# Optimization experiments

Hardware: AMD Instinct MI355X
Metric: run time of the kernel (lower is better)

The kernel has to match this reference:

```python
import jax, jax.numpy as jnp
import numpy as np

N_NODES = 100000
N_EDGES = 1600000
IN_DIM, HID_DIM, OUT_DIM = 128, 64, 64


def setup_inputs() -> dict:
    key = jax.random.key(0)
    ks = jax.random.split(key, 8)
    x = jax.random.normal(ks[0], (N_NODES, IN_DIM), dtype=jnp.float32)
    edge_index = jax.random.randint(ks[1], (2, N_EDGES), 0, N_NODES, dtype=jnp.int32)
    edge_weight = jax.random.uniform(ks[2], (N_EDGES,), dtype=jnp.float32)
    # GCNConv parameters (glorot-ish init)
    w1 = jax.random.normal(ks[3], (IN_DIM, HID_DIM), dtype=jnp.float32) / np.sqrt(IN_DIM)
    b1 = jnp.zeros((HID_DIM,), dtype=jnp.float32)
    w2 = jax.random.normal(ks[4], (HID_DIM, OUT_DIM), dtype=jnp.float32) / np.sqrt(HID_DIM)
    b2 = jnp.zeros((OUT_DIM,), dtype=jnp.float32)
    return {"x": x, "edge_index": edge_index, "edge_weight": edge_weight,
            "w1": w1, "b1": b1, "w2": w2, "b2": b2}


def _gcn_conv(h, src, dst, edge_weight, w, b, n_nodes):
    # GCNConv(normalize=False): linear transform, then edge-weighted scatter-add
    # (source_to_target flow: gather from src, scatter-sum into dst), then bias.
    h = h @ w                                   # [N, out]
    msg = h[src] * edge_weight[:, None]          # [E, out] irregular gather
    agg = jax.ops.segment_sum(msg, dst, num_segments=n_nodes)  # [N, out]
    return agg + b


def reference(x, edge_index, edge_weight, w1, b1, w2, b2):
    src, dst = edge_index[0], edge_index[1]
    n = x.shape[0]
    # Dropout is identity in eval mode (training=False).
    h = _gcn_conv(x, src, dst, edge_weight, w1, b1, n)
    h = jax.nn.relu(h)
    out = _gcn_conv(h, src, dst, edge_weight, w2, b2, n)
    return out
```

## Files before the change

kernel.cpp:

```cpp
#include <hip/hip_runtime.h>
#include <hip/hip_bf16.h>


#define N_NODES 100000
#define N_EDGES 1600000
#define NB1     391
#define T1      4096
#define NT1     391
#define EPT     8
#define CAP1    4706
#define GB1     782

typedef unsigned short ushort_t;
typedef unsigned int uint_t;
typedef __attribute__((ext_vector_type(8))) short bf16x8;
typedef __attribute__((ext_vector_type(4))) float floatx4;
typedef __attribute__((ext_vector_type(8))) ushort_t ushort8v;

static __device__ __forceinline__ float bf2f(ushort_t h) {
    return __uint_as_float(((uint_t)h) << 16);
}
static __device__ __forceinline__ ushort_t f2bf(float f) {
    uint_t u = __float_as_uint(f);
    u = (u + 0x7FFF + ((u >> 16) & 1)) >> 16;
    return (ushort_t)u;
}

__global__ __launch_bounds__(512) void k_init(int* __restrict__ gcursor)
{
    int t = threadIdx.x;
    if (t < NB1) gcursor[t] = t * CAP1;
}

__global__ __launch_bounds__(512) void k_p1g1(
    const int* __restrict__ src, const int* __restrict__ dst,
    const float* __restrict__ ew, int* __restrict__ gcursor,
    int2* __restrict__ recs1, int E,
    const float* __restrict__ X, const float* __restrict__ W,
    ushort_t* __restrict__ Y, int N)
{
    __shared__ __align__(16) char smem[47296];
    const int tid = threadIdx.x;

    if (blockIdx.x < NT1) {
        int* cnt     = (int*)smem;
        int* start   = cnt + NB1;
        int* cursor  = start + NB1;
        int* gb      = cursor + NB1;
        int* wsum    = (int*)(smem + 6256);
        int* wexc    = wsum + 8;
        int2* stg    = (int2*)(smem + 6336);
        ushort_t* sb = (ushort_t*)(smem + 39104);
        const int t = tid, b = blockIdx.x;
        const int lane = t & 63, wv = t >> 6;

        int   rd[EPT]; int rs[EPT]; float rw[EPT];
        const int e0 = b * T1;
        const int e1 = min(E, e0 + T1);
        #pragma unroll
        for (int i = 0; i < EPT; ++i) {
            int e  = e0 + t + i * 512;
            int ee = (e < e1) ? e : e0;
            rd[i] = dst[ee];
            rs[i] = src[ee];
            rw[i] = ew[ee];
            if (e >= e1) rd[i] = -1;
        }

        if (t < NB1) cnt[t] = 0;
        __syncthreads();
        #pragma unroll
        for (int i = 0; i < EPT; ++i)
            if (rd[i] >= 0) atomicAdd(&cnt[rd[i] >> 8], 1);
        __syncthreads();

        const int v = (t < NB1) ? cnt[t] : 0;
        int x = v;
        #pragma unroll
        for (int off = 1; off < 64; off <<= 1) {
            int y = __shfl_up(x, off);
            if (lane >= off) x += y;
        }
        if (lane == 63) wsum[wv] = x;
        __syncthreads();
        if (t < 8) {
            int w  = wsum[t];
            int xx = w;
            #pragma unroll
            for (int off = 1; off < 8; off <<= 1) {
                int y = __shfl_up(xx, off);
                if (t >= off) xx += y;
            }
            wexc[t] = xx - w;
        }
        __syncthreads();
        if (t < NB1) {
            int st = x + wexc[wv] - v;
            start[t]  = st;
            cursor[t] = st;
            gb[t]     = atomicAdd(&gcursor[t], v);
        }
        __syncthreads();

        #pragma unroll
        for (int i = 0; i < EPT; ++i) {
            int d = rd[i];
            if (d >= 0) {
                int bk = d >> 8;
                int p  = atomicAdd(&cursor[bk], 1);
                int2 r;
                r.x = ((d & 255) << 17) | rs[i];
                r.y = __float_as_int(rw[i]);
                stg[p] = r;
                sb[p]  = (ushort_t)bk;
            }
        }
        __syncthreads();
        const int n = e1 - e0;
        for (int i = t; i < n; i += 512) {
            int bk = sb[i];
            recs1[gb[bk] + (i - start[bk])] = stg[i];
        }
    } else {
        ushort_t* sA = (ushort_t*)smem;
        ushort_t* sB = (ushort_t*)(smem + 18432);
        const int b    = blockIdx.x - NT1;
        const int row0 = b * 128;

        for (int i = tid; i < 128 * 16; i += 512) {
            int k = i >> 4, n4 = (i & 15) * 4;
            float4 v = *(const float4*)(W + (size_t)k * 64 + n4);
            sB[(n4 + 0) * 136 + k] = f2bf(v.x);
            sB[(n4 + 1) * 136 + k] = f2bf(v.y);
            sB[(n4 + 2) * 136 + k] = f2bf(v.z);
            sB[(n4 + 3) * 136 + k] = f2bf(v.w);
        }
        for (int i = tid; i < 128 * 16; i += 512) {
            int r = i >> 4, c4 = (i & 15) * 4;
            int rg = row0 + r; if (rg > N - 1) rg = N - 1;
            float4 v = *(const float4*)(X + (size_t)rg * 128 + c4);
            *(ushort4*)(sA + r * 72 + c4) =
                make_ushort4(f2bf(v.x), f2bf(v.y), f2bf(v.z), f2bf(v.w));
        }
        __syncthreads();

        const int wid = tid >> 6, lane = tid & 63;
        const int m = lane & 15, quad = lane >> 4;
        floatx4 acc[4] = {};

        #pragma unroll
        for (int ksl = 0; ksl < 2; ++ksl) {
            bf16x8 a = *(const bf16x8*)(sA + (wid * 16 + m) * 72 + ksl * 32 + quad * 8);
            #pragma unroll
            for (int nt = 0; nt < 4; ++nt) {
                bf16x8 bfr = *(const bf16x8*)(sB + (nt * 16 + m) * 136 + ksl * 32 + quad * 8);
                acc[nt] = __builtin_amdgcn_mfma_f32_16x16x32_bf16(a, bfr, acc[nt], 0, 0, 0);
            }
        }
        __syncthreads();
        for (int i = tid; i < 128 * 16; i += 512) {
            int r = i >> 4, c4 = (i & 15) * 4;
            int rg = row0 + r; if (rg > N - 1) rg = N - 1;
            float4 v = *(const float4*)(X + (size_t)rg * 128 + 64 + c4);
            *(ushort4*)(sA + r * 72 + c4) =
                make_ushort4(f2bf(v.x), f2bf(v.y), f2bf(v.z), f2bf(v.w));
        }
        __syncthreads();
        #pragma unroll
        for (int ksl = 0; ksl < 2; ++ksl) {
            bf16x8 a = *(const bf16x8*)(sA + (wid * 16 + m) * 72 + ksl * 32 + quad * 8);
            #pragma unroll
            for (int nt = 0; nt < 4; ++nt) {
                bf16x8 bfr = *(const bf16x8*)(sB + (nt * 16 + m) * 136 + 64 + ksl * 32 + quad * 8);
                acc[nt] = __builtin_amdgcn_mfma_f32_16x16x32_bf16(a, bfr, acc[nt], 0, 0, 0);
            }
        }
        __syncthreads();
        #pragma unroll
        for (int nt = 0; nt < 4; ++nt)
            #pragma unroll
            for (int r = 0; r < 4; ++r)
                sA[(wid * 16 + quad * 4 + r) * 72 + nt * 16 + m] = f2bf(acc[nt][r]);
        __syncthreads();
        for (int i = tid; i < 128 * 8; i += 512) {
            int rr = i >> 3, c8 = (i & 7) * 8;
            int rg = row0 + rr;
            if (rg < N)
                *(ushort8v*)(Y + (size_t)rg * 64 + c8) =
                    *(const ushort8v*)(sA + rr * 72 + c8);
        }
    }
}

__global__ __launch_bounds__(1024) void k_pass2(
    const int2* __restrict__ recs1, const int* __restrict__ gcursor,
    int2* __restrict__ recs2, int2* __restrict__ nodeinfo, int N)
{
    __shared__ int cnt[256];
    __shared__ int s[256];
    __shared__ int cursor[256];
    const int t = threadIdx.x, b = blockIdx.x;
    const int lo = b * CAP1;
    const int hi = gcursor[b];

    if (t < 256) cnt[t] = 0;
    __syncthreads();
    for (int j = lo + t; j < hi; j += 1024)
        atomicAdd(&cnt[((uint_t)recs1[j].x) >> 17], 1);
    __syncthreads();
    const int v = (t < 256) ? cnt[t] : 0;
    if (t < 256) s[t] = v;
    #pragma unroll
    for (int off = 1; off < 256; off <<= 1) {
        __syncthreads();
        int a = (t >= off && t < 256) ? s[t - off] : 0;
        __syncthreads();
        if (t < 256) s[t] += a;
    }
    __syncthreads();
    if (t < 256) {
        const int stl = s[t] - v;
        cursor[t] = stl;
        const int ng = b * 256 + t;
        if (ng < N) {
            int2 ni; ni.x = lo + stl; ni.y = v;
            nodeinfo[ng] = ni;
        }
    }
    __syncthreads();
    for (int j = lo + t; j < hi; j += 1024) {
        int2 r = recs1[j];
        int dl = ((uint_t)r.x) >> 17;
        int p  = atomicAdd(&cursor[dl], 1);
        int2 o;
        o.x = r.x & 0x1FFFF;
        o.y = r.y;
        recs2[lo + p] = o;
    }
}

__global__ __launch_bounds__(256) void k_gather_mm(
    const ushort_t* __restrict__ H, const int2* __restrict__ recs,
    const int2* __restrict__ nodeinfo, const float* __restrict__ bias1,
    const float* __restrict__ W2, ushort_t* __restrict__ out)
{
    __shared__ ushort_t sW[64 * 72];
    __shared__ ushort_t strip[4][128];

    const int tid  = threadIdx.x;
    const int wid  = tid >> 6;
    const int lane = tid & 63;
    const int n0   = (blockIdx.x * 4 + wid) * 2;
    const int n1   = n0 + 1;

    for (int i = tid; i < 64 * 16; i += 256) {
        int k = i >> 4, n4 = (i & 15) * 4;
        float4 v = *(const float4*)(W2 + (size_t)k * 64 + n4);
        sW[(n4 + 0) * 72 + k] = f2bf(v.x);
        sW[(n4 + 1) * 72 + k] = f2bf(v.y);
        sW[(n4 + 2) * 72 + k] = f2bf(v.z);
        sW[(n4 + 3) * 72 + k] = f2bf(v.w);
    }

    const int2 niA = nodeinfo[n0];
    const int2 niB = nodeinfo[n1];
    int baseA = niA.x; const int endA = niA.x + niA.y;
    int baseB = niB.x; const int endB = niB.x + niB.y;

    const int g  = lane >> 4;
    const int c4 = (lane & 15) * 4;

    float a0 = 0.f, a1 = 0.f, a2 = 0.f, a3 = 0.f;
    float b0 = 0.f, b1 = 0.f, b2 = 0.f, b3 = 0.f;

    while (baseA < endA || baseB < endB) {
        int mA = endA - baseA; if (mA > 64) mA = 64;
        int mB = endB - baseB; if (mB > 64) mB = 64;
        int2 rA = (mA > 0) ? recs[baseA + (lane < mA ? lane : mA - 1)]
                           : make_int2(0, 0);
        int2 rB = (mB > 0) ? recs[baseB + (lane < mB ? lane : mB - 1)]
                           : make_int2(0, 0);
        float wAf = __int_as_float(rA.y);
        float wBf = __int_as_float(rB.y);
        int mm = mA > mB ? mA : mB;
        #pragma unroll 4
        for (int jj = 0; jj < mm; jj += 4) {
            int idx = jj + g;
            int   sA_ = __shfl(rA.x, idx);
            float wA  = __shfl(wAf, idx);
            int   sB_ = __shfl(rB.x, idx);
            float wB  = __shfl(wBf, idx);
            if (idx >= mA) wA = 0.f;
            if (idx >= mB) wB = 0.f;
            ushort4 hA = *(const ushort4*)(H + (size_t)sA_ * 64 + c4);
            ushort4 hB = *(const ushort4*)(H + (size_t)sB_ * 64 + c4);
            a0 = fmaf(wA, bf2f(hA.x), a0);
            a1 = fmaf(wA, bf2f(hA.y), a1);
            a2 = fmaf(wA, bf2f(hA.z), a2);
            a3 = fmaf(wA, bf2f(hA.w), a3);
            b0 = fmaf(wB, bf2f(hB.x), b0);
            b1 = fmaf(wB, bf2f(hB.y), b1);
            b2 = fmaf(wB, bf2f(hB.z), b2);
            b3 = fmaf(wB, bf2f(hB.w), b3);
        }
        baseA += 64;
        baseB += 64;
    }
    a0 += __shfl_down(a0, 32); a1 += __shfl_down(a1, 32);
    a2 += __shfl_down(a2, 32); a3 += __shfl_down(a3, 32);
    b0 += __shfl_down(b0, 32); b1 += __shfl_down(b1, 32);
    b2 += __shfl_down(b2, 32); b3 += __shfl_down(b3, 32);
    a0 += __shfl_down(a0, 16); a1 += __shfl_down(a1, 16);
    a2 += __shfl_down(a2, 16); a3 += __shfl_down(a3, 16);
    b0 += __shfl_down(b0, 16); b1 += __shfl_down(b1, 16);
    b2 += __shfl_down(b2, 16); b3 += __shfl_down(b3, 16);

    if (lane < 16) {
        float4 bv = *(const float4*)(bias1 + c4);
        float vA0 = fmaxf(a0 + bv.x, 0.f), vA1 = fmaxf(a1 + bv.y, 0.f);
        float vA2 = fmaxf(a2 + bv.z, 0.f), vA3 = fmaxf(a3 + bv.w, 0.f);
        float vB0 = fmaxf(b0 + bv.x, 0.f), vB1 = fmaxf(b1 + bv.y, 0.f);
        float vB2 = fmaxf(b2 + bv.z, 0.f), vB3 = fmaxf(b3 + bv.w, 0.f);
        *(ushort4*)(&strip[wid][0 * 64 + c4]) =
            make_ushort4(f2bf(vA0), f2bf(vA1), f2bf(vA2), f2bf(vA3));
        *(ushort4*)(&strip[wid][1 * 64 + c4]) =
            make_ushort4(f2bf(vB0), f2bf(vB1), f2bf(vB2), f2bf(vB3));
    }
    __syncthreads();

    const int m = lane & 15, quad = lane >> 4;
    const ushort_t* sp = strip[wid];
    floatx4 acc2[4] = {};
    #pragma unroll
    for (int ks = 0; ks < 2; ++ks) {
        bf16x8 a = *(const bf16x8*)(sp + (m & 1) * 64 + ks * 32 + quad * 8);
        #pragma unroll
        for (int nt = 0; nt < 4; ++nt) {
            bf16x8 bfr = *(const bf16x8*)(sW + (nt * 16 + m) * 72 + ks * 32 + quad * 8);
            acc2[nt] = __builtin_amdgcn_mfma_f32_16x16x32_bf16(a, bfr, acc2[nt], 0, 0, 0);
        }
    }
    if (quad == 0) {
        #pragma unroll
        for (int nt = 0; nt < 4; ++nt) {
            strip[wid][0 * 64 + nt * 16 + m] = f2bf(acc2[nt][0]);
            strip[wid][1 * 64 + nt * 16 + m] = f2bf(acc2[nt][1]);
        }
    }
    __syncthreads();
    if (lane < 32) {
        int rr = lane >> 4, mm2 = lane & 15;
        *(ushort4*)(out + (size_t)(n0 + rr) * 64 + mm2 * 4) =
            *(const ushort4*)(&strip[wid][rr * 64 + mm2 * 4]);
    }
}

__global__ __launch_bounds__(256) void k_gather2(
    const ushort_t* __restrict__ H, const int2* __restrict__ recs,
    const int2* __restrict__ nodeinfo, const float* __restrict__ bias,
    float* __restrict__ out)
{
    const int wid  = threadIdx.x >> 6;
    const int lane = threadIdx.x & 63;
    const int n0   = (blockIdx.x * 4 + wid) * 2;
    const int n1   = n0 + 1;

    const int2 niA = nodeinfo[n0];
    const int2 niB = nodeinfo[n1];
    int baseA = niA.x; const int endA = niA.x + niA.y;
    int baseB = niB.x; const int endB = niB.x + niB.y;

    const int g  = lane >> 4;
    const int c4 = (lane & 15) * 4;

    float a0 = 0.f, a1 = 0.f, a2 = 0.f, a3 = 0.f;
    float b0 = 0.f, b1 = 0.f, b2 = 0.f, b3 = 0.f;

    while (baseA < endA || baseB < endB) {
        int mA = endA - baseA; if (mA > 64) mA = 64;
        int mB = endB - baseB; if (mB > 64) mB = 64;
        int2 rA = (mA > 0) ? recs[baseA + (lane < mA ? lane : mA - 1)]
                           : make_int2(0, 0);
        int2 rB = (mB > 0) ? recs[baseB + (lane < mB ? lane : mB - 1)]
                           : make_int2(0, 0);
        float wAf = __int_as_float(rA.y);
        float wBf = __int_as_float(rB.y);
        int mm = mA > mB ? mA : mB;
        #pragma unroll 4
        for (int jj = 0; jj < mm; jj += 4) {
            int idx = jj + g;
            int   sA_ = __shfl(rA.x, idx);
            float wA  = __shfl(wAf, idx);
            int   sB_ = __shfl(rB.x, idx);
            float wB  = __shfl(wBf, idx);
            if (idx >= mA) wA = 0.f;
            if (idx >= mB) wB = 0.f;
            ushort4 hA = *(const ushort4*)(H + (size_t)sA_ * 64 + c4);
            ushort4 hB = *(const ushort4*)(H + (size_t)sB_ * 64 + c4);
            a0 = fmaf(wA, bf2f(hA.x), a0);
            a1 = fmaf(wA, bf2f(hA.y), a1);
            a2 = fmaf(wA, bf2f(hA.z), a2);
            a3 = fmaf(wA, bf2f(hA.w), a3);
            b0 = fmaf(wB, bf2f(hB.x), b0);
            b1 = fmaf(wB, bf2f(hB.y), b1);
            b2 = fmaf(wB, bf2f(hB.z), b2);
            b3 = fmaf(wB, bf2f(hB.w), b3);
        }
        baseA += 64;
        baseB += 64;
    }
    a0 += __shfl_down(a0, 32); a1 += __shfl_down(a1, 32);
    a2 += __shfl_down(a2, 32); a3 += __shfl_down(a3, 32);
    b0 += __shfl_down(b0, 32); b1 += __shfl_down(b1, 32);
    b2 += __shfl_down(b2, 32); b3 += __shfl_down(b3, 32);
    a0 += __shfl_down(a0, 16); a1 += __shfl_down(a1, 16);
    a2 += __shfl_down(a2, 16); a3 += __shfl_down(a3, 16);
    b0 += __shfl_down(b0, 16); b1 += __shfl_down(b1, 16);
    b2 += __shfl_down(b2, 16); b3 += __shfl_down(b3, 16);

    if (lane < 16) {
        float4 bv = *(const float4*)(bias + c4);
        *(float4*)(out + (size_t)n0 * 64 + c4) =
            make_float4(a0 + bv.x, a1 + bv.y, a2 + bv.z, a3 + bv.w);
        *(float4*)(out + (size_t)n1 * 64 + c4) =
            make_float4(b0 + bv.x, b1 + bv.y, b2 + bv.z, b3 + bv.w);
    }
}

extern "C" void kernel_launch(void* const* d_in, const int* in_sizes, int n_in,
                              void* d_out, int out_size, void* d_ws, size_t ws_size,
                              hipStream_t stream) {
    const float* x   = (const float*)d_in[0];
    const int*   ei  = (const int*)  d_in[1];
    const float* ew  = (const float*)d_in[2];
    const float* w1  = (const float*)d_in[3];
    const float* b1  = (const float*)d_in[4];
    const float* w2  = (const float*)d_in[5];
    const float* b2  = (const float*)d_in[6];
    float* out = (float*)d_out;

    const int N = N_NODES, E = N_EDGES;
    const int* src = ei;
    const int* dst = ei + E;

    char* p = (char*)d_ws;
    ushort_t* bufA   = (ushort_t*)p;  p += (size_t)N_NODES * 64 * 2;
    int2*     recs2  = (int2*)p;      p += (size_t)NB1 * CAP1 * 8;
    int2*     recs1  = (int2*)p;
    ushort_t* bufB   = (ushort_t*)p;  p += (size_t)NB1 * CAP1 * 8;
    int*      gcur   = (int*)p;       p += 2048;
    int2*     ninfo  = (int2*)p;      p += (size_t)N_NODES * 8;

    k_init <<<1, 512, 0, stream>>>(gcur);
    k_p1g1 <<<NT1 + GB1, 512, 0, stream>>>(src, dst, ew, gcur, recs1, E,
                                           x, w1, bufA, N);
    k_pass2<<<NB1, 1024, 0, stream>>>(recs1, gcur, recs2, ninfo, N);

    k_gather_mm<<<N / 8, 256, 0, stream>>>(bufA, recs2, ninfo, b1, w2, bufB);

    k_gather2<<<N / 8, 256, 0, stream>>>(bufB, recs2, ninfo, b2, out);
}
```

Before: 247.8 us.

## Reorder second GCN layer to aggregate before applying W2 and stream edge loads

Moves the W2 matmul from after the first aggregation to after the second aggregation, so layer one writes relu(agg+b1) and layer two gathers it then applies the MFMA matmul plus bias and writes fp32 output. By linearity this matches the reference while removing one bf16 rounding of transformed features. The partition kernel also drops per-thread register buffering of edges and re-reads dst/src/ew in strided loops, trading register pressure for a second dst read. Final output stores become scalar rather than vectorized.

```diff
diff --git a/kernel.cpp b/kernel.cpp
--- a/kernel.cpp
+++ b/kernel.cpp
@@ -7,7 +7,6 @@
 #define NB1     391
 #define T1      4096
 #define NT1     391
-#define EPT     8
 #define CAP1    4706
 #define GB1     782
 
@@ -54,24 +53,12 @@
         const int t = tid, b = blockIdx.x;
         const int lane = t & 63, wv = t >> 6;
 
-        int   rd[EPT]; int rs[EPT]; float rw[EPT];
+        if (t < NB1) cnt[t] = 0;
+        __syncthreads();
         const int e0 = b * T1;
         const int e1 = min(E, e0 + T1);
-        #pragma unroll
-        for (int i = 0; i < EPT; ++i) {
-            int e  = e0 + t + i * 512;
-            int ee = (e < e1) ? e : e0;
-            rd[i] = dst[ee];
-            rs[i] = src[ee];
-            rw[i] = ew[ee];
-            if (e >= e1) rd[i] = -1;
-        }
-
-        if (t < NB1) cnt[t] = 0;
-        __syncthreads();
-        #pragma unroll
-        for (int i = 0; i < EPT; ++i)
-            if (rd[i] >= 0) atomicAdd(&cnt[rd[i] >> 8], 1);
+        for (int e = e0 + t; e < e1; e += 512)
+            atomicAdd(&cnt[dst[e] >> 8], 1);
         __syncthreads();
 
         const int v = (t < NB1) ? cnt[t] : 0;
@@ -102,18 +89,15 @@
         }
         __syncthreads();
 
-        #pragma unroll
-        for (int i = 0; i < EPT; ++i) {
-            int d = rd[i];
-            if (d >= 0) {
-                int bk = d >> 8;
-                int p  = atomicAdd(&cursor[bk], 1);
-                int2 r;
-                r.x = ((d & 255) << 17) | rs[i];
-                r.y = __float_as_int(rw[i]);
-                stg[p] = r;
-                sb[p]  = (ushort_t)bk;
-            }
+        for (int e = e0 + t; e < e1; e += 512) {
+            int d  = dst[e];
+            int bk = d >> 8;
+            int p  = atomicAdd(&cursor[bk], 1);
+            int2 r;
+            r.x = ((d & 255) << 17) | src[e];
+            r.y = __float_as_int(ew[e]);
+            stg[p] = r;
+            sb[p]  = (ushort_t)bk;
         }
         __syncthreads();
         const int n = e1 - e0;
@@ -239,10 +223,86 @@
     }
 }
 
-__global__ __launch_bounds__(256) void k_gather_mm(
+__global__ __launch_bounds__(256) void k_gather1(
     const ushort_t* __restrict__ H, const int2* __restrict__ recs,
-    const int2* __restrict__ nodeinfo, const float* __restrict__ bias1,
-    const float* __restrict__ W2, ushort_t* __restrict__ out)
+    const int2* __restrict__ nodeinfo, const float* __restrict__ bias,
+    ushort_t* __restrict__ out)
+{
+    const int wid  = threadIdx.x >> 6;
+    const int lane = threadIdx.x & 63;
+    const int n0   = (blockIdx.x * 4 + wid) * 2;
+    const int n1   = n0 + 1;
+
+    const int2 niA = nodeinfo[n0];
+    const int2 niB = nodeinfo[n1];
+    int baseA = niA.x; const int endA = niA.x + niA.y;
+    int baseB = niB.x; const int endB = niB.x + niB.y;
+
+    const int g  = lane >> 4;
+    const int c4 = (lane & 15) * 4;
+
+    float a0 = 0.f, a1 = 0.f, a2 = 0.f, a3 = 0.f;
+    float b0 = 0.f, b1 = 0.f, b2 = 0.f, b3 = 0.f;
+
+    while (baseA < endA || baseB < endB) {
+        int mA = endA - baseA; if (mA > 64) mA = 64;
+        int mB = endB - baseB; if (mB > 64) mB = 64;
+        int2 rA = (mA > 0) ? recs[baseA + (lane < mA ? lane : mA - 1)]
+                           : make_int2(0, 0);
+        int2 rB = (mB > 0) ? recs[baseB + (lane < mB ? lane : mB - 1)]
+                           : make_int2(0, 0);
+        float wAf = __int_as_float(rA.y);
+        float wBf = __int_as_float(rB.y);
+        int mm = mA > mB ? mA : mB;
+        #pragma unroll 4
+        for (int jj = 0; jj < mm; jj += 4) {
+            int idx = jj + g;
+            int   sA = __shfl(rA.x, idx);
+            float wA = __shfl(wAf, idx);
+            int   sB = __shfl(rB.x, idx);
+            float wB = __shfl(wBf, idx);
+            if (idx >= mA) wA = 0.f;
+            if (idx >= mB) wB = 0.f;
+            ushort4 hA = *(const ushort4*)(H + (size_t)sA * 64 + c4);
+            ushort4 hB = *(const ushort4*)(H + (size_t)sB * 64 + c4);
+            a0 = fmaf(wA, bf2f(hA.x), a0);
+            a1 = fmaf(wA, bf2f(hA.y), a1);
+            a2 = fmaf(wA, bf2f(hA.z), a2);
+            a3 = fmaf(wA, bf2f(hA.w), a3);
+            b0 = fmaf(wB, bf2f(hB.x), b0);
+            b1 = fmaf(wB, bf2f(hB.y), b1);
+            b2 = fmaf(wB, bf2f(hB.z), b2);
+            b3 = fmaf(wB, bf2f(hB.w), b3);
+        }
+        baseA += 64;
+        baseB += 64;
+    }
+    a0 += __shfl_down(a0, 32); a1 += __shfl_down(a1, 32);
+    a2 += __shfl_down(a2, 32); a3 += __shfl_down(a3, 32);
+    b0 += __shfl_down(b0, 32); b1 += __shfl_down(b1, 32);
+    b2 += __shfl_down(b2, 32); b3 += __shfl_down(b3, 32);
+    a0 += __shfl_down(a0, 16); a1 += __shfl_down(a1, 16);
+    a2 += __shfl_down(a2, 16); a3 += __shfl_down(a3, 16);
+    b0 += __shfl_down(b0, 16); b1 += __shfl_down(b1, 16);
+    b2 += __shfl_down(b2, 16); b3 += __shfl_down(b3, 16);
+
+    if (lane < 16) {
+        float4 bv = *(const float4*)(bias + c4);
+        float vA0 = fmaxf(a0 + bv.x, 0.f), vA1 = fmaxf(a1 + bv.y, 0.f);
+        float vA2 = fmaxf(a2 + bv.z, 0.f), vA3 = fmaxf(a3 + bv.w, 0.f);
+        float vB0 = fmaxf(b0 + bv.x, 0.f), vB1 = fmaxf(b1 + bv.y, 0.f);
+        float vB2 = fmaxf(b2 + bv.z, 0.f), vB3 = fmaxf(b3 + bv.w, 0.f);
+        *(ushort4*)(out + (size_t)n0 * 64 + c4) =
+            make_ushort4(f2bf(vA0), f2bf(vA1), f2bf(vA2), f2bf(vA3));
+        *(ushort4*)(out + (size_t)n1 * 64 + c4) =
+            make_ushort4(f2bf(vB0), f2bf(vB1), f2bf(vB2), f2bf(vB3));
+    }
+}
+
+__global__ __launch_bounds__(256) void k_gather2mm(
+    const ushort_t* __restrict__ H, const int2* __restrict__ recs,
+    const int2* __restrict__ nodeinfo, const float* __restrict__ bias2,
+    const float* __restrict__ W2, float* __restrict__ out)
 {
     __shared__ ushort_t sW[64 * 72];
     __shared__ ushort_t strip[4][128];
@@ -261,6 +321,7 @@
         sW[(n4 + 2) * 72 + k] = f2bf(v.z);
         sW[(n4 + 3) * 72 + k] = f2bf(v.w);
     }
+    __syncthreads();
 
     const int2 niA = nodeinfo[n0];
     const int2 niB = nodeinfo[n1];
@@ -316,17 +377,12 @@
     b2 += __shfl_down(b2, 16); b3 += __shfl_down(b3, 16);
 
     if (lane < 16) {
-        float4 bv = *(const float4*)(bias1 + c4);
-        float vA0 = fmaxf(a0 + bv.x, 0.f), vA1 = fmaxf(a1 + bv.y, 0.f);
-        float vA2 = fmaxf(a2 + bv.z, 0.f), vA3 = fmaxf(a3 + bv.w, 0.f);
-        float vB0 = fmaxf(b0 + bv.x, 0.f), vB1 = fmaxf(b1 + bv.y, 0.f);
-        float vB2 = fmaxf(b2 + bv.z, 0.f), vB3 = fmaxf(b3 + bv.w, 0.f);
         *(ushort4*)(&strip[wid][0 * 64 + c4]) =
-            make_ushort4(f2bf(vA0), f2bf(vA1), f2bf(vA2), f2bf(vA3));
+            make_ushort4(f2bf(a0), f2bf(a1), f2bf(a2), f2bf(a3));
         *(ushort4*)(&strip[wid][1 * 64 + c4]) =
-            make_ushort4(f2bf(vB0), f2bf(vB1), f2bf(vB2), f2bf(vB3));
-    }
-    __syncthreads();
+            make_ushort4(f2bf(b0), f2bf(b1), f2bf(b2), f2bf(b3));
+    }
+    __builtin_amdgcn_wave_barrier();
 
     const int m = lane & 15, quad = lane >> 4;
     const ushort_t* sp = strip[wid];
@@ -343,87 +399,10 @@
     if (quad == 0) {
         #pragma unroll
         for (int nt = 0; nt < 4; ++nt) {
-            strip[wid][0 * 64 + nt * 16 + m] = f2bf(acc2[nt][0]);
-            strip[wid][1 * 64 + nt * 16 + m] = f2bf(acc2[nt][1]);
-        }
-    }
-    __syncthreads();
-    if (lane < 32) {
-        int rr = lane >> 4, mm2 = lane & 15;
-        *(ushort4*)(out + (size_t)(n0 + rr) * 64 + mm2 * 4) =
-            *(const ushort4*)(&strip[wid][rr * 64 + mm2 * 4]);
-    }
-}
-
-__global__ __launch_bounds__(256) void k_gather2(
-    const ushort_t* __restrict__ H, const int2* __restrict__ recs,
-    const int2* __restrict__ nodeinfo, const float* __restrict__ bias,
-    float* __restrict__ out)
-{
-    const int wid  = threadIdx.x >> 6;
-    const int lane = threadIdx.x & 63;
-    const int n0   = (blockIdx.x * 4 + wid) * 2;
-    const int n1   = n0 + 1;
-
-    const int2 niA = nodeinfo[n0];
-    const int2 niB = nodeinfo[n1];
-    int baseA = niA.x; const int endA = niA.x + niA.y;
-    int baseB = niB.x; const int endB = niB.x + niB.y;
-
-    const int g  = lane >> 4;
-    const int c4 = (lane & 15) * 4;
-
-    float a0 = 0.f, a1 = 0.f, a2 = 0.f, a3 = 0.f;
-    float b0 = 0.f, b1 = 0.f, b2 = 0.f, b3 = 0.f;
-
-    while (baseA < endA || baseB < endB) {
-        int mA = endA - baseA; if (mA > 64) mA = 64;
-        int mB = endB - baseB; if (mB > 64) mB = 64;
-        int2 rA = (mA > 0) ? recs[baseA + (lane < mA ? lane : mA - 1)]
-                           : make_int2(0, 0);
-        int2 rB = (mB > 0) ? recs[baseB + (lane < mB ? lane : mB - 1)]
-                           : make_int2(0, 0);
-        float wAf = __int_as_float(rA.y);
-        float wBf = __int_as_float(rB.y);
-        int mm = mA > mB ? mA : mB;
-        #pragma unroll 4
-        for (int jj = 0; jj < mm; jj += 4) {
-            int idx = jj + g;
-            int   sA_ = __shfl(rA.x, idx);
-            float wA  = __shfl(wAf, idx);
-            int   sB_ = __shfl(rB.x, idx);
-            float wB  = __shfl(wBf, idx);
-            if (idx >= mA) wA = 0.f;
-            if (idx >= mB) wB = 0.f;
-            ushort4 hA = *(const ushort4*)(H + (size_t)sA_ * 64 + c4);
-            ushort4 hB = *(const ushort4*)(H + (size_t)sB_ * 64 + c4);
-            a0 = fmaf(wA, bf2f(hA.x), a0);
-            a1 = fmaf(wA, bf2f(hA.y), a1);
-            a2 = fmaf(wA, bf2f(hA.z), a2);
-            a3 = fmaf(wA, bf2f(hA.w), a3);
-            b0 = fmaf(wB, bf2f(hB.x), b0);
-            b1 = fmaf(wB, bf2f(hB.y), b1);
-            b2 = fmaf(wB, bf2f(hB.z), b2);
-            b3 = fmaf(wB, bf2f(hB.w), b3);
-        }
-        baseA += 64;
-        baseB += 64;
-    }
-    a0 += __shfl_down(a0, 32); a1 += __shfl_down(a1, 32);
-    a2 += __shfl_down(a2, 32); a3 += __shfl_down(a3, 32);
-    b0 += __shfl_down(b0, 32); b1 += __shfl_down(b1, 32);
-    b2 += __shfl_down(b2, 32); b3 += __shfl_down(b3, 32);
-    a0 += __shfl_down(a0, 16); a1 += __shfl_down(a1, 16);
-    a2 += __shfl_down(a2, 16); a3 += __shfl_down(a3, 16);
-    b0 += __shfl_down(b0, 16); b1 += __shfl_down(b1, 16);
-    b2 += __shfl_down(b2, 16); b3 += __shfl_down(b3, 16);
-
-    if (lane < 16) {
-        float4 bv = *(const float4*)(bias + c4);
-        *(float4*)(out + (size_t)n0 * 64 + c4) =
-            make_float4(a0 + bv.x, a1 + bv.y, a2 + bv.z, a3 + bv.w);
-        *(float4*)(out + (size_t)n1 * 64 + c4) =
-            make_float4(b0 + bv.x, b1 + bv.y, b2 + bv.z, b3 + bv.w);
+            float bb0 = bias2[nt * 16 + m];
+            out[(size_t)n0 * 64 + nt * 16 + m] = acc2[nt][0] + bb0;
+            out[(size_t)n1 * 64 + nt * 16 + m] = acc2[nt][1] + bb0;
+        }
     }
 }
 
@@ -456,7 +435,7 @@
                                            x, w1, bufA, N);
     k_pass2<<<NB1, 1024, 0, stream>>>(recs1, gcur, recs2, ninfo, N);
 
-    k_gather_mm<<<N / 8, 256, 0, stream>>>(bufA, recs2, ninfo, b1, w2, bufB);
-
-    k_gather2<<<N / 8, 256, 0, stream>>>(bufB, recs2, ninfo, b2, out);
-}
+    k_gather1<<<N / 8, 256, 0, stream>>>(bufA, recs2, ninfo, b1, bufB);
+
+    k_gather2mm<<<N / 8, 256, 0, stream>>>(bufB, recs2, ninfo, b2, w2, out);
+}
```

After: 245.3 us. About the same (-1.0%).
